# Kernel tuning notes

Measured on AMD Instinct MI355X. Metric: run time of the kernel, lower is better.

Reference implementation:

```python
import jax, jax.numpy as jnp
import numpy as np
from jax import lax

N, M, D, K = 65536, 16, 128, 8
DD = D // K  # delta_d


def _normalize(x, axis):
    # torch F.normalize: x / max(||x||_2, 1e-12)
    return x / jnp.maximum(jnp.linalg.norm(x, axis=axis, keepdims=True), 1e-12)


def setup_inputs() -> dict:
    key0 = jax.random.key(0)
    k1, k2, k3, k4 = jax.random.split(key0, 4)
    h = jax.random.normal(k1, (N, D), dtype=jnp.float32)
    neighbors = jax.random.randint(k2, (N * M,), 0, N)
    stdv = 1.0 / np.sqrt(DD)
    query = jax.random.uniform(k3, (DD, DD), minval=-stdv, maxval=stdv, dtype=jnp.float32)
    key_w = jax.random.uniform(k4, (DD, DD), minval=-stdv, maxval=stdv, dtype=jnp.float32)
    return {"h": h, "neighbors": neighbors, "query": query, "key_w": key_w,
            "iterat": 3, "max_iter": 10}


def _calc_prob(x, centre, cov):
    # x: [n,1,dd], centre: [n,k,dd], cov: [n,k,dd]
    dd = centre.shape[-1]
    diff = x - centre  # [n,k,dd]
    log_result = jnp.log(cov)
    log_result = jnp.where(jnp.isnan(log_result), jnp.float32(1e-6), log_result)
    # double-log as in the original (may produce NaN for negative log_result)
    dets = jnp.exp(jnp.sum(jnp.log(log_result), axis=2))  # [n,k]
    coef = jnp.float32(1.0 / np.sqrt((2.0 * np.pi) ** dd / 2.0))
    left = coef / jnp.sqrt(dets + 1e-6)  # [n,k]
    # diff @ diag(cov) @ diff^T == sum(cov * diff^2)
    right = jnp.exp(-0.5 * jnp.sum(cov * diff * diff, axis=2))  # [n,k]
    prob = left * right
    prob = _normalize(prob, axis=1)
    prob = jnp.where(jnp.isnan(prob), jnp.float32(1e-6), prob)
    return prob


def _forward(h, neighbors, query, key_w, iterat):
    n, d = h.shape
    dd = query.shape[0]
    k = d // dd
    m = neighbors.shape[0] // n
    nb = h[neighbors].reshape(n, m, k, dd)  # neighbor gather [n,m,k,dd]
    hc = _normalize(h.reshape(n, k, dd), axis=2)  # per-capsule normalized [n,k,dd]
    q = jnp.einsum('nke,ef->nkf', hc, query)
    kk = jnp.einsum('nke,ef->nkf', hc, key_w)
    # diagonal of q @ kk^T over capsules
    att_logit = jnp.einsum('nke,nke->nk', q, kk)
    att = jax.nn.softmax(att_logit, axis=1)[..., None]  # [n,k,1]

    # ---- calcCovs (no grad in original) ----
    qs = jnp.einsum('nmke,ef->nmkf', nb, query)  # [n,m,k,dd]
    # sum over neighbors of (qs @ kk^T): [n,k,k]
    p_matrix = jnp.einsum('nmkf,njf->nkj', qs, kk)
    diagv = jnp.diagonal(p_matrix, axis1=1, axis2=2)  # [n,k]
    # torch quirk: p[i] = torch.diag(p_matrix[i]) broadcasts the diag vector across rows
    p_b = jnp.broadcast_to(diagv[:, None, :], (n, k, k))
    sub = jnp.concatenate([nb, hc[:, None]], axis=1)  # [n,m+1,k,dd]
    sub = jnp.transpose(sub, (0, 2, 1, 3))  # [n,k,m+1,dd]
    sub = _normalize(sub, axis=2)  # normalize along neighbor axis
    L = m + 1
    # torch.median returns the lower median -> sorted element at (L-1)//2
    middle = jnp.sort(sub, axis=2)[:, :, (L - 1) // 2, :]  # [n,k,dd]
    cov = jnp.einsum('nij,njd->nid', p_b, (hc - middle) ** 2)  # [n,k,dd]
    cov = lax.stop_gradient(cov)

    # ---- iterative routing ----
    ix = jnp.sum(att * hc, axis=1, keepdims=True)  # [n,1,dd]
    for _ in range(iterat):
        p = lax.stop_gradient(_calc_prob(ix, hc, cov))[..., None]  # [n,k,1]
        ix = jnp.sum(att * p * hc, axis=1, keepdims=True) / (
            jnp.sum(att * p, axis=1, keepdims=True) + 1e-9)
    x = _normalize(ix[:, 0, :], axis=1)  # [n,dd]
    return x, att[..., 0]


def reference(h, neighbors, query, key_w, iterat, max_iter):
    del max_iter  # unused in the original forward
    return _forward(h, neighbors, query, key_w, iterat)
```

## Files before the change

### kernel.cpp

```cpp
#include <hip/hip_runtime.h>
#include <hip/hip_bf16.h>

#define MD 128
#define KC 8
#define KD 16
#define MN 16
#define QS 20

typedef _Float16 f16x2 __attribute__((ext_vector_type(2)));

static __device__ __forceinline__ float lo_bf(unsigned int w){ union{unsigned int i;float f;}c; c.i=w<<16;        return c.f; }
static __device__ __forceinline__ float hi_bf(unsigned int w){ union{unsigned int i;float f;}c; c.i=w&0xffff0000u; return c.f; }
static __device__ __forceinline__ float bf2f1(unsigned short u){ union{unsigned int i;float f;}c; c.i=((unsigned int)u)<<16; return c.f; }

template<bool BF>
static __device__ __forceinline__ float load1(const void* base, int off) {
    if (BF) return bf2f1(((const unsigned short*)base)[off]);
    return ((const float*)base)[off];
}

static __device__ __forceinline__ float fast_rsq(float x){ return __builtin_amdgcn_rsqf(x); }
static __device__ __forceinline__ float fast_rcp(float x){ return __builtin_amdgcn_rcpf(x); }

static __device__ __forceinline__ unsigned phmin(unsigned a, unsigned b) {
    return __builtin_bit_cast(unsigned, __builtin_elementwise_min(
        __builtin_bit_cast(f16x2, a), __builtin_bit_cast(f16x2, b)));
}
static __device__ __forceinline__ unsigned phmax(unsigned a, unsigned b) {
    return __builtin_bit_cast(unsigned, __builtin_elementwise_max(
        __builtin_bit_cast(f16x2, a), __builtin_bit_cast(f16x2, b)));
}
static __device__ __forceinline__ void pcas(unsigned& x, unsigned& y) {
    unsigned lo = phmin(x, y), hi = phmax(x, y); x = lo; y = hi;
}
static __device__ __forceinline__ void psort8(unsigned a[8]) {
    pcas(a[0],a[1]); pcas(a[2],a[3]); pcas(a[4],a[5]); pcas(a[6],a[7]);
    pcas(a[0],a[2]); pcas(a[1],a[3]); pcas(a[4],a[6]); pcas(a[5],a[7]);
    pcas(a[1],a[2]); pcas(a[5],a[6]);
    pcas(a[0],a[4]); pcas(a[2],a[6]); pcas(a[2],a[4]);
    pcas(a[1],a[5]); pcas(a[3],a[7]); pcas(a[3],a[5]);
    pcas(a[1],a[2]); pcas(a[3],a[4]); pcas(a[5],a[6]);
}
static __device__ __forceinline__ void pmed16(unsigned a[16], unsigned& b7, unsigned& b8) {
    psort8(a); psort8(a + 8);
    const unsigned* u = a; const unsigned* v = a + 8;
    unsigned t7 =             phmin(u[7], v[0]);
    t7 = phmax(t7, phmin(u[6], v[1]));
    t7 = phmax(t7, phmin(u[5], v[2]));
    t7 = phmax(t7, phmin(u[4], v[3]));
    t7 = phmax(t7, phmin(u[3], v[4]));
    t7 = phmax(t7, phmin(u[2], v[5]));
    t7 = phmax(t7, phmin(u[1], v[6]));
    t7 = phmax(t7, phmin(u[0], v[7]));
    unsigned t8 = phmax(u[0], v[0]);
    t8 = phmax(t8, phmin(u[7], v[1]));
    t8 = phmax(t8, phmin(u[6], v[2]));
    t8 = phmax(t8, phmin(u[5], v[3]));
    t8 = phmax(t8, phmin(u[4], v[4]));
    t8 = phmax(t8, phmin(u[3], v[5]));
    t8 = phmax(t8, phmin(u[2], v[6]));
    t8 = phmax(t8, phmin(u[1], v[7]));
    b7 = t7; b8 = t8;
}

static __device__ __forceinline__ void cas(float& x, float& y) {
    float lo = fminf(x, y), hi = fmaxf(x, y); x = lo; y = hi;
}
static __device__ __forceinline__ void sort8f(float a[8]) {
    cas(a[0],a[1]); cas(a[2],a[3]); cas(a[4],a[5]); cas(a[6],a[7]);
    cas(a[0],a[2]); cas(a[1],a[3]); cas(a[4],a[6]); cas(a[5],a[7]);
    cas(a[1],a[2]); cas(a[5],a[6]);
    cas(a[0],a[4]); cas(a[2],a[6]); cas(a[2],a[4]);
    cas(a[1],a[5]); cas(a[3],a[7]); cas(a[3],a[5]);
    cas(a[1],a[2]); cas(a[3],a[4]); cas(a[5],a[6]);
}
static __device__ __forceinline__ float med17f(float a[16], float self) {
    sort8f(a); sort8f(a + 8);
    const float* u = a; const float* v = a + 8;
    float t7 =            fminf(u[7], v[0]);
    t7 = fmaxf(t7, fminf(u[6], v[1])); t7 = fmaxf(t7, fminf(u[5], v[2]));
    t7 = fmaxf(t7, fminf(u[4], v[3])); t7 = fmaxf(t7, fminf(u[3], v[4]));
    t7 = fmaxf(t7, fminf(u[2], v[5])); t7 = fmaxf(t7, fminf(u[1], v[6]));
    t7 = fmaxf(t7, fminf(u[0], v[7]));
    float t8 = fmaxf(u[0], v[0]);
    t8 = fmaxf(t8, fminf(u[7], v[1])); t8 = fmaxf(t8, fminf(u[6], v[2]));
    t8 = fmaxf(t8, fminf(u[5], v[3])); t8 = fmaxf(t8, fminf(u[4], v[4]));
    t8 = fmaxf(t8, fminf(u[3], v[5])); t8 = fmaxf(t8, fminf(u[2], v[6]));
    t8 = fmaxf(t8, fminf(u[1], v[7]));
    return __builtin_amdgcn_fmed3f(self, t7, t8);
}

template<int CTRL>
static __device__ __forceinline__ float dpp_mov(float v) {
    return __int_as_float(__builtin_amdgcn_update_dpp(
        0, __float_as_int(v), CTRL, 0xF, 0xF, false));
}
static __device__ __forceinline__ float rsum_quad(float v) {
    v += dpp_mov<0xB1>(v);
    v += dpp_mov<0x4E>(v);
    return v;
}
static __device__ __forceinline__ float rsum_caps(float v) {
    v += __shfl_xor(v, 4);
    v += dpp_mov<0x128>(v);
    v += __shfl_xor(v, 16);
    return v;
}
static __device__ __forceinline__ float rmax_caps(float v) {
    v = fmaxf(v, __shfl_xor(v, 4));
    v = fmaxf(v, dpp_mov<0x128>(v));
    v = fmaxf(v, __shfl_xor(v, 16));
    return v;
}

__global__ void detect_dtype(const unsigned short* __restrict__ h, int* __restrict__ flag) {
    int l = threadIdx.x;
    float m = 0.f;
    for (int i = l; i < 1024; i += 64) {
        float v = bf2f1(h[i]);
        v = (v != v) ? 1e30f : fabsf(v);
        m = fmaxf(m, v);
    }
    #pragma unroll
    for (int off = 1; off < 64; off <<= 1) m = fmaxf(m, __shfl_xor(m, off));
    if (l == 0) flag[0] = (m < 1000.0f) ? 1 : 0;
}

template<bool BF>
__global__ __launch_bounds__(256)
void attn_fwd(const void* __restrict__ hraw,
              const int* __restrict__ nbr,
              const void* __restrict__ qry,
              const void* __restrict__ keyw,
              const int* __restrict__ iterat_p,
              const int* __restrict__ flag_p,
              void* __restrict__ out,
              int n_nodes)
{
    if (flag_p[0] != (BF ? 1 : 0)) return;

    const int tid  = threadIdx.x;
    const int wid  = tid >> 6;
    const int l    = tid & 63;
    const int sub  = l & 31;
    const int half = (l >> 5) & 1;
    const int k    = sub >> 2;
    const int q4   = sub & 3;

    int n = blockIdx.x * 8 + wid * 2 + half;
    if (n >= n_nodes) n = n_nodes - 1;

    __shared__ float qs[16 * QS];
    __shared__ float kts[16 * QS];
    {
        float qv = load1<BF>(qry, tid);
        float kv = load1<BF>(keyw, tid);
        int e = tid >> 4, f = tid & 15;
        qs [e * QS + f] = qv;
        kts[f * QS + e] = kv;
    }

    int nnb = blockIdx.x * 8 + wid * 2 + ((l >> 4) & 1);
    if (nnb >= n_nodes) nnb = n_nodes - 1;
    const int nbv = nbr[nnb * MN + (l & 15)];

    float hp[4];
    if (BF) {
        uint2 w0 = ((const uint2*)hraw)[(size_t)n * 32 + sub];
        hp[0] = lo_bf(w0.x); hp[1] = hi_bf(w0.x); hp[2] = lo_bf(w0.y); hp[3] = hi_bf(w0.y);
    } else {
        float4 t = ((const float4*)hraw)[(size_t)n * 32 + sub];
        hp[0] = t.x; hp[1] = t.y; hp[2] = t.z; hp[3] = t.w;
    }
    float ss = 0;
    #pragma unroll
    for (int i = 0; i < 4; ++i) ss = fmaf(hp[i], hp[i], ss);
    ss = rsum_quad(ss);
    float inv = fast_rsq(fmaxf(ss, 1e-24f));
    float hc[4];
    #pragma unroll
    for (int i = 0; i < 4; ++i) hc[i] = hp[i] * inv;

    __syncthreads();

    const int vb = half << 6;
    uint2  rb[16]; float4 rf[16];
    #pragma unroll
    for (int m = 0; m < MN; ++m) {
        int idx = __builtin_amdgcn_ds_bpermute(vb + m * 4, nbv);
        if (BF) rb[m] = *(const uint2*) ((const char*)hraw + (((unsigned)idx << 8) + (unsigned)sub * 8u));
        else    rf[m] = *(const float4*)((const char*)hraw + (((unsigned)idx << 9) + (unsigned)sub * 16u));
    }

    float hcA[4][4];
    #pragma unroll
    for (int j = 0; j < 4; ++j) {
        hcA[0][j] = dpp_mov<0x00>(hc[j]);
        hcA[1][j] = dpp_mov<0x55>(hc[j]);
        hcA[2][j] = dpp_mov<0xAA>(hc[j]);
        hcA[3][j] = dpp_mov<0xFF>(hc[j]);
    }
    float kk[4];
    #pragma unroll
    for (int i = 0; i < 4; ++i) {
        const float* row = &kts[(q4 * 4 + i) * QS];
        float acc = 0;
        #pragma unroll
        for (int r = 0; r < 4; ++r) {
            float4 kr = *(const float4*)(row + r * 4);
            acc = fmaf(hcA[r][0], kr.x, acc);
            acc = fmaf(hcA[r][1], kr.y, acc);
            acc = fmaf(hcA[r][2], kr.z, acc);
            acc = fmaf(hcA[r][3], kr.w, acc);
        }
        kk[i] = acc;
    }
    float kkA[4][4];
    #pragma unroll
    for (int j = 0; j < 4; ++j) {
        kkA[0][j] = dpp_mov<0x00>(kk[j]);
        kkA[1][j] = dpp_mov<0x55>(kk[j]);
        kkA[2][j] = dpp_mov<0xAA>(kk[j]);
        kkA[3][j] = dpp_mov<0xFF>(kk[j]);
    }
    float w[4];
    #pragma unroll
    for (int i = 0; i < 4; ++i) {
        const float* row = &qs[(q4 * 4 + i) * QS];
        float acc = 0;
        #pragma unroll
        for (int r = 0; r < 4; ++r) {
            float4 qr = *(const float4*)(row + r * 4);
            acc = fmaf(kkA[r][0], qr.x, acc);
            acc = fmaf(kkA[r][1], qr.y, acc);
            acc = fmaf(kkA[r][2], qr.z, acc);
            acc = fmaf(kkA[r][3], qr.w, acc);
        }
        w[i] = acc;
    }

    float lg = 0;
    #pragma unroll
    for (int i = 0; i < 4; ++i) lg = fmaf(hc[i], w[i], lg);
    float logit = rsum_quad(lg);
    float mx  = rmax_caps(logit);
    float ex  = __expf(logit - mx);
    float att = ex * fast_rcp(rsum_caps(ex));

    float sn[4] = {0,0,0,0}, s2[4] = {0,0,0,0};
    #pragma unroll
    for (int m = 0; m < 16; ++m) {
        float x0, x1, x2, x3;
        if (BF) { x0=lo_bf(rb[m].x); x1=hi_bf(rb[m].x); x2=lo_bf(rb[m].y); x3=hi_bf(rb[m].y); }
        else    { x0=rf[m].x; x1=rf[m].y; x2=rf[m].z; x3=rf[m].w; }
        sn[0]+=x0; sn[1]+=x1; sn[2]+=x2; sn[3]+=x3;
        s2[0]=fmaf(x0,x0,s2[0]); s2[1]=fmaf(x1,x1,s2[1]);
        s2[2]=fmaf(x2,x2,s2[2]); s2[3]=fmaf(x3,x3,s2[3]);
    }

    float mid[4];
    if (BF) {
        unsigned a[16];
        #pragma unroll
        for (int m = 0; m < 16; ++m) a[m] = rb[m].x;
        unsigned b7, b8; pmed16(a, b7, b8);
        mid[0] = __builtin_amdgcn_fmed3f(hc[0], lo_bf(b7), lo_bf(b8));
        mid[1] = __builtin_amdgcn_fmed3f(hc[1], hi_bf(b7), hi_bf(b8));
        #pragma unroll
        for (int m = 0; m < 16; ++m) a[m] = rb[m].y;
        pmed16(a, b7, b8);
        mid[2] = __builtin_amdgcn_fmed3f(hc[2], lo_bf(b7), lo_bf(b8));
        mid[3] = __builtin_amdgcn_fmed3f(hc[3], hi_bf(b7), hi_bf(b8));
    } else {
        #pragma unroll
        for (int c = 0; c < 4; ++c) {
            float a[16];
            #pragma unroll
            for (int m = 0; m < 16; ++m)
                a[m] = (c==0) ? rf[m].x : (c==1) ? rf[m].y : (c==2) ? rf[m].z : rf[m].w;
            mid[c] = med17f(a, hc[c]);
        }
    }
    #pragma unroll
    for (int c = 0; c < 4; ++c) {
        float t2 = fmaf(hc[c], hc[c], s2[c]);
        mid[c] *= fast_rsq(fmaxf(t2, 1e-24f));
    }

    float dgl = 0;
    #pragma unroll
    for (int i = 0; i < 4; ++i) dgl = fmaf(sn[i], w[i], dgl);
    float dg = rsum_quad(dgl);

    float cv[4];
    #pragma unroll
    for (int i = 0; i < 4; ++i) {
        float t = hc[i] - mid[i];
        cv[i] = rsum_caps(dg * t * t);
    }

    float lsl = 0;
    #pragma unroll
    for (int i = 0; i < 4; ++i) {
        float lr = __logf(cv[i]);
        lr = (lr != lr) ? 1e-6f : lr;
        lsl += __logf(lr);
    }
    float ls   = rsum_quad(lsl);
    float dets = __expf(ls);
    const float coef = 5.822108e-7f;
    float left = coef * fast_rsq(dets + 1e-6f);

    float ah[4], ix[4];
    #pragma unroll
    for (int i = 0; i < 4; ++i) ah[i] = att * hc[i];
    #pragma unroll
    for (int i = 0; i < 4; ++i) ix[i] = rsum_caps(ah[i]);

    const int iterat = iterat_p[0];
    for (int it = 0; it < iterat; ++it) {
        float rsl = 0;
        #pragma unroll
        for (int i = 0; i < 4; ++i) {
            float df = ix[i] - hc[i];
            rsl = fmaf(cv[i] * df, df, rsl);
        }
        float rs   = rsum_quad(rsl);
        float prob = left * __expf(-0.5f * rs);
        float p2   = rsum_caps(prob * prob);
        float pn   = prob * fast_rsq(fmaxf(p2, 1e-24f));
        pn = (pn != pn) ? 1e-6f : pn;
        float den = rsum_caps(att * pn);
        float num[4];
        #pragma unroll
        for (int i = 0; i < 4; ++i) num[i] = rsum_caps(pn * ah[i]);
        float rr = fast_rcp(den + 1e-9f);
        #pragma unroll
        for (int i = 0; i < 4; ++i) ix[i] = num[i] * rr;
    }

    float xs = 0;
    #pragma unroll
    for (int i = 0; i < 4; ++i) xs = fmaf(ix[i], ix[i], xs);
    xs = rsum_quad(xs);
    float xinv = fast_rsq(fmaxf(xs, 1e-24f));

    if (BF) {
        if (sub < 4) {
            __hip_bfloat16 b0 = __float2bfloat16(ix[0] * xinv);
            __hip_bfloat16 b1 = __float2bfloat16(ix[1] * xinv);
            __hip_bfloat16 b2 = __float2bfloat16(ix[2] * xinv);
            __hip_bfloat16 b3 = __float2bfloat16(ix[3] * xinv);
            uint2 o;
            o.x = (unsigned)(*(unsigned short*)&b0) | ((unsigned)(*(unsigned short*)&b1) << 16);
            o.y = (unsigned)(*(unsigned short*)&b2) | ((unsigned)(*(unsigned short*)&b3) << 16);
            *(uint2*)((char*)out + (size_t)n * 32 + q4 * 8) = o;
        }
        if (q4 == 0) {
            __hip_bfloat16 ba = __float2bfloat16(att);
            ((unsigned short*)out)[(size_t)n_nodes * KD + (size_t)n * KC + k] =
                *(unsigned short*)&ba;
        }
    } else {
        if (sub < 4) {
            float4 o;
            o.x = ix[0] * xinv; o.y = ix[1] * xinv; o.z = ix[2] * xinv; o.w = ix[3] * xinv;
            *(float4*)((float*)out + (size_t)n * KD + q4 * 4) = o;
        }
        if (q4 == 0) ((float*)out)[(size_t)n_nodes * KD + (size_t)n * KC + k] = att;
    }
}

extern "C" void kernel_launch(void* const* d_in, const int* in_sizes, int n_in,
                              void* d_out, int out_size, void* d_ws, size_t ws_size,
                              hipStream_t stream) {
    const void* h    = d_in[0];
    const int*  nbr  = (const int*)d_in[1];
    const void* qry  = d_in[2];
    const void* keyw = (const void*)d_in[3];
    const int*  iterat_p = (const int*)d_in[4];

    int n_nodes = in_sizes[0] / MD;
    int* flag = (int*)d_ws;

    detect_dtype<<<1, 64, 0, stream>>>((const unsigned short*)h, flag);

    int blocks = (n_nodes + 7) / 8;
    attn_fwd<true ><<<blocks, 256, 0, stream>>>(h, nbr, qry, keyw, iterat_p, flag, d_out, n_nodes);
    attn_fwd<false><<<blocks, 256, 0, stream>>>(h, nbr, qry, keyw, iterat_p, flag, d_out, n_nodes);
}
```

Before: 87.13 us.

## Inline dtype detection per wave and drop separate detect kernel launch

Removes the single-wave detect_dtype kernel and has every wave of both template instances read the first 256 bf16 words of h and reduce a max-abs to decide which variant proceeds. This removes one kernel launch and its serial dependency, at the cost of a small redundant load and reduction per wave. It also replaces a shfl_xor with a row-shift DPP in the capsule reductions and enables bound_ctrl on DPP moves. It splits the gathered bf16 rows into separate x/y arrays so the median sort runs on them without copying, and hoists the iterat load to the top of the kernel.

```diff
diff --git a/kernel.cpp b/kernel.cpp
--- a/kernel.cpp
+++ b/kernel.cpp
@@ -21,6 +21,30 @@
 
 static __device__ __forceinline__ float fast_rsq(float x){ return __builtin_amdgcn_rsqf(x); }
 static __device__ __forceinline__ float fast_rcp(float x){ return __builtin_amdgcn_rcpf(x); }
+
+template<int CTRL>
+static __device__ __forceinline__ float dpp_mov(float v) {
+    return __int_as_float(__builtin_amdgcn_update_dpp(
+        0, __float_as_int(v), CTRL, 0xF, 0xF, true));
+}
+
+static __device__ __forceinline__ float rsum_quad(float v) {
+    v += dpp_mov<0xB1>(v);
+    v += dpp_mov<0x4E>(v);
+    return v;
+}
+static __device__ __forceinline__ float rsum_caps(float v) {
+    v += dpp_mov<0x124>(v);
+    v += dpp_mov<0x128>(v);
+    v += __shfl_xor(v, 16);
+    return v;
+}
+static __device__ __forceinline__ float rmax_caps(float v) {
+    v = fmaxf(v, dpp_mov<0x124>(v));
+    v = fmaxf(v, dpp_mov<0x128>(v));
+    v = fmaxf(v, __shfl_xor(v, 16));
+    return v;
+}
 
 static __device__ __forceinline__ unsigned phmin(unsigned a, unsigned b) {
     return __builtin_bit_cast(unsigned, __builtin_elementwise_min(
@@ -90,42 +114,6 @@
     return __builtin_amdgcn_fmed3f(self, t7, t8);
 }
 
-template<int CTRL>
-static __device__ __forceinline__ float dpp_mov(float v) {
-    return __int_as_float(__builtin_amdgcn_update_dpp(
-        0, __float_as_int(v), CTRL, 0xF, 0xF, false));
-}
-static __device__ __forceinline__ float rsum_quad(float v) {
-    v += dpp_mov<0xB1>(v);
-    v += dpp_mov<0x4E>(v);
-    return v;
-}
-static __device__ __forceinline__ float rsum_caps(float v) {
-    v += __shfl_xor(v, 4);
-    v += dpp_mov<0x128>(v);
-    v += __shfl_xor(v, 16);
-    return v;
-}
-static __device__ __forceinline__ float rmax_caps(float v) {
-    v = fmaxf(v, __shfl_xor(v, 4));
-    v = fmaxf(v, dpp_mov<0x128>(v));
-    v = fmaxf(v, __shfl_xor(v, 16));
-    return v;
-}
-
-__global__ void detect_dtype(const unsigned short* __restrict__ h, int* __restrict__ flag) {
-    int l = threadIdx.x;
-    float m = 0.f;
-    for (int i = l; i < 1024; i += 64) {
-        float v = bf2f1(h[i]);
-        v = (v != v) ? 1e30f : fabsf(v);
-        m = fmaxf(m, v);
-    }
-    #pragma unroll
-    for (int off = 1; off < 64; off <<= 1) m = fmaxf(m, __shfl_xor(m, off));
-    if (l == 0) flag[0] = (m < 1000.0f) ? 1 : 0;
-}
-
 template<bool BF>
 __global__ __launch_bounds__(256)
 void attn_fwd(const void* __restrict__ hraw,
@@ -133,12 +121,9 @@
               const void* __restrict__ qry,
               const void* __restrict__ keyw,
               const int* __restrict__ iterat_p,
-              const int* __restrict__ flag_p,
               void* __restrict__ out,
               int n_nodes)
 {
-    if (flag_p[0] != (BF ? 1 : 0)) return;
-
     const int tid  = threadIdx.x;
     const int wid  = tid >> 6;
     const int l    = tid & 63;
@@ -146,6 +131,24 @@
     const int half = (l >> 5) & 1;
     const int k    = sub >> 2;
     const int q4   = sub & 3;
+
+    const int iterat = iterat_p[0];
+
+    {
+        uint2 w = ((const uint2*)hraw)[l];
+        float a0 = fabsf(lo_bf(w.x)); a0 = (a0 != a0) ? 1e30f : a0;
+        float a1 = fabsf(hi_bf(w.x)); a1 = (a1 != a1) ? 1e30f : a1;
+        float a2 = fabsf(lo_bf(w.y)); a2 = (a2 != a2) ? 1e30f : a2;
+        float a3 = fabsf(hi_bf(w.y)); a3 = (a3 != a3) ? 1e30f : a3;
+        float m = fmaxf(fmaxf(a0, a1), fmaxf(a2, a3));
+        m = fmaxf(m, dpp_mov<0xB1>(m));
+        m = fmaxf(m, dpp_mov<0x4E>(m));
+        m = fmaxf(m, dpp_mov<0x124>(m));
+        m = fmaxf(m, dpp_mov<0x128>(m));
+        m = fmaxf(m, __shfl_xor(m, 16));
+        m = fmaxf(m, __shfl_xor(m, 32));
+        if ((m < 1000.0f) != BF) return;
+    }
 
     int n = blockIdx.x * 8 + wid * 2 + half;
     if (n >= n_nodes) n = n_nodes - 1;
@@ -184,12 +187,16 @@
     __syncthreads();
 
     const int vb = half << 6;
-    uint2  rb[16]; float4 rf[16];
+    unsigned rbx[16], rby[16]; float4 rf[16];
     #pragma unroll
     for (int m = 0; m < MN; ++m) {
         int idx = __builtin_amdgcn_ds_bpermute(vb + m * 4, nbv);
-        if (BF) rb[m] = *(const uint2*) ((const char*)hraw + (((unsigned)idx << 8) + (unsigned)sub * 8u));
-        else    rf[m] = *(const float4*)((const char*)hraw + (((unsigned)idx << 9) + (unsigned)sub * 16u));
+        if (BF) {
+            uint2 t = *(const uint2*)((const char*)hraw + (((unsigned)idx << 8) + (unsigned)sub * 8u));
+            rbx[m] = t.x; rby[m] = t.y;
+        } else {
+            rf[m] = *(const float4*)((const char*)hraw + (((unsigned)idx << 9) + (unsigned)sub * 16u));
+        }
     }
 
     float hcA[4][4];
@@ -251,7 +258,7 @@
     #pragma unroll
     for (int m = 0; m < 16; ++m) {
         float x0, x1, x2, x3;
-        if (BF) { x0=lo_bf(rb[m].x); x1=hi_bf(rb[m].x); x2=lo_bf(rb[m].y); x3=hi_bf(rb[m].y); }
+        if (BF) { x0=lo_bf(rbx[m]); x1=hi_bf(rbx[m]); x2=lo_bf(rby[m]); x3=hi_bf(rby[m]); }
         else    { x0=rf[m].x; x1=rf[m].y; x2=rf[m].z; x3=rf[m].w; }
         sn[0]+=x0; sn[1]+=x1; sn[2]+=x2; sn[3]+=x3;
         s2[0]=fmaf(x0,x0,s2[0]); s2[1]=fmaf(x1,x1,s2[1]);
@@ -260,15 +267,11 @@
 
     float mid[4];
     if (BF) {
-        unsigned a[16];
-        #pragma unroll
-        for (int m = 0; m < 16; ++m) a[m] = rb[m].x;
-        unsigned b7, b8; pmed16(a, b7, b8);
+        unsigned b7, b8;
+        pmed16(rbx, b7, b8);
         mid[0] = __builtin_amdgcn_fmed3f(hc[0], lo_bf(b7), lo_bf(b8));
         mid[1] = __builtin_amdgcn_fmed3f(hc[1], hi_bf(b7), hi_bf(b8));
-        #pragma unroll
-        for (int m = 0; m < 16; ++m) a[m] = rb[m].y;
-        pmed16(a, b7, b8);
+        pmed16(rby, b7, b8);
         mid[2] = __builtin_amdgcn_fmed3f(hc[2], lo_bf(b7), lo_bf(b8));
         mid[3] = __builtin_amdgcn_fmed3f(hc[3], hi_bf(b7), hi_bf(b8));
     } else {
@@ -317,7 +320,6 @@
     #pragma unroll
     for (int i = 0; i < 4; ++i) ix[i] = rsum_caps(ah[i]);
 
-    const int iterat = iterat_p[0];
     for (int it = 0; it < iterat; ++it) {
         float rsl = 0;
         #pragma unroll
@@ -381,11 +383,8 @@
     const int*  iterat_p = (const int*)d_in[4];
 
     int n_nodes = in_sizes[0] / MD;
-    int* flag = (int*)d_ws;
-
-    detect_dtype<<<1, 64, 0, stream>>>((const unsigned short*)h, flag);
 
     int blocks = (n_nodes + 7) / 8;
-    attn_fwd<true ><<<blocks, 256, 0, stream>>>(h, nbr, qry, keyw, iterat_p, flag, d_out, n_nodes);
-    attn_fwd<false><<<blocks, 256, 0, stream>>>(h, nbr, qry, keyw, iterat_p, flag, d_out, n_nodes);
-}
+    attn_fwd<true ><<<blocks, 256, 0, stream>>>(h, nbr, qry, keyw, iterat_p, d_out, n_nodes);
+    attn_fwd<false><<<blocks, 256, 0, stream>>>(h, nbr, qry, keyw, iterat_p, d_out, n_nodes);
+}
```

After: 88.40 us. About the same (+1.4%).
